# Kernel optimization log

Measured on AMD Instinct MI355X. Metric: run time of the kernel, lower is better.

The kernel has to match this reference:

```python
import jax, jax.numpy as jnp
import numpy as np

B, H, W, C = 32, 64, 64, 256
NH, WS, SHIFT = 8, 8, 4
HD = C // NH
N = WS * WS           # tokens per window
NW = (H // WS) * (W // WS)
HID = 4 * C
EPS_LN = 1e-5
LOGIT_MAX = float(np.log(1.0 / 0.01))


def _rel_coords_table():
    ch = np.arange(-(WS - 1), WS, dtype=np.float32)
    t = np.stack(np.meshgrid(ch, ch, indexing='ij'), axis=-1)  # (2WS-1, 2WS-1, 2)
    t = t / (WS - 1) * 8.0
    t = np.sign(t) * np.log2(np.abs(t) + 1.0) / np.log2(8.0)
    return t.reshape(-1, 2)  # ((2WS-1)^2, 2)


def _rel_pos_index():
    coords = np.stack(np.meshgrid(np.arange(WS), np.arange(WS), indexing='ij'))
    cf = coords.reshape(2, -1)
    rel = (cf[:, :, None] - cf[:, None, :]).transpose(1, 2, 0).copy()
    rel[:, :, 0] += WS - 1
    rel[:, :, 1] += WS - 1
    rel[:, :, 0] *= 2 * WS - 1
    return rel.sum(-1)  # (N, N) int


def _attn_mask():
    img = np.zeros((H, W), np.float32)
    cnt = 0
    for hs in (slice(0, -WS), slice(-WS, -SHIFT), slice(-SHIFT, None)):
        for ws in (slice(0, -WS), slice(-WS, -SHIFT), slice(-SHIFT, None)):
            img[hs, ws] = cnt
            cnt += 1
    mw = img.reshape(H // WS, WS, W // WS, WS).transpose(0, 2, 1, 3).reshape(-1, N)
    diff = mw[:, None, :] - mw[:, :, None]
    return np.where(diff != 0, -100.0, 0.0).astype(np.float32)  # (NW, N, N)


_RCT = jnp.asarray(_rel_coords_table())
_RPI = jnp.asarray(_rel_pos_index())
_MASK = jnp.asarray(_attn_mask())


def _ln(x, g, b):
    mu = jnp.mean(x, axis=-1, keepdims=True)
    var = jnp.mean(jnp.square(x - mu), axis=-1, keepdims=True)
    return (x - mu) * jax.lax.rsqrt(var + EPS_LN) * g + b


def _l2n(x):
    return x / jnp.sqrt(jnp.maximum(jnp.sum(x * x, axis=-1, keepdims=True), 1e-12))


def setup_inputs() -> dict:
    key = jax.random.key(0)
    ks = jax.random.split(key, 16)
    s = 0.02
    return {
        'x': jax.random.normal(ks[0], (B, H * W, C), jnp.float32),
        'qkv_w': jax.random.normal(ks[1], (C, 3 * C), jnp.float32) * s,
        'q_bias': jnp.zeros((C,), jnp.float32),
        'v_bias': jnp.zeros((C,), jnp.float32),
        'logit_scale': jnp.full((NH, 1, 1), np.log(10.0), jnp.float32),
        'cpb_w1': jax.random.normal(ks[2], (2, 512), jnp.float32) * s,
        'cpb_b1': jnp.zeros((512,), jnp.float32),
        'cpb_w2': jax.random.normal(ks[3], (512, NH), jnp.float32) * s,
        'proj_w': jax.random.normal(ks[4], (C, C), jnp.float32) * s,
        'proj_b': jnp.zeros((C,), jnp.float32),
        'norm1_g': jnp.ones((C,), jnp.float32),
        'norm1_b': jnp.zeros((C,), jnp.float32),
        'fc1_w': jax.random.normal(ks[5], (C, HID), jnp.float32) * s,
        'fc1_b': jnp.zeros((HID,), jnp.float32),
        'fc2_w': jax.random.normal(ks[6], (HID, C), jnp.float32) * s,
        'fc2_b': jnp.zeros((C,), jnp.float32),
        'norm2_g': jnp.ones((C,), jnp.float32),
        'norm2_b': jnp.zeros((C,), jnp.float32),
    }


def reference(x, qkv_w, q_bias, v_bias, logit_scale, cpb_w1, cpb_b1, cpb_w2,
              proj_w, proj_b, norm1_g, norm1_b, fc1_w, fc1_b, fc2_w, fc2_b,
              norm2_g, norm2_b):
    shortcut = x
    xs = x.reshape(B, H, W, C)
    # cyclic shift
    xs = jnp.roll(xs, shift=(-SHIFT, -SHIFT), axis=(1, 2))
    # window partition -> (B*NW, N, C)
    xw = xs.reshape(B, H // WS, WS, W // WS, WS, C).transpose(0, 1, 3, 2, 4, 5)
    xw = xw.reshape(B * NW, N, C)

    # qkv projection (kernel without bias, then split q/v biases, k bias zero)
    qkv_bias = jnp.concatenate([q_bias, jnp.zeros_like(q_bias), v_bias], axis=0)
    qkv = xw @ qkv_w + qkv_bias
    qkv = qkv.reshape(B * NW, N, 3, NH, HD).transpose(2, 0, 3, 1, 4)
    q, k, v = qkv[0], qkv[1], qkv[2]  # (B*NW, NH, N, HD)

    # cosine attention
    attn = jnp.einsum('bhnd,bhmd->bhnm', _l2n(q), _l2n(k))
    scale = jnp.exp(jnp.minimum(logit_scale, LOGIT_MAX))  # (NH,1,1)
    attn = attn * scale

    # CPB-MLP relative position bias
    table = jax.nn.relu(_RCT @ cpb_w1 + cpb_b1) @ cpb_w2          # ((2WS-1)^2, NH)
    bias = table[_RPI]                                            # (N, N, NH)
    bias = 16.0 * jax.nn.sigmoid(bias.transpose(2, 0, 1))         # (NH, N, N)
    attn = attn + bias[None]

    # shifted-window mask
    attn = attn.reshape(B, NW, NH, N, N) + _MASK[None, :, None]
    attn = jax.nn.softmax(attn.reshape(B * NW, NH, N, N), axis=-1)

    out = jnp.einsum('bhnm,bhmd->bhnd', attn, v)
    out = out.transpose(0, 2, 1, 3).reshape(B * NW, N, C)
    out = out @ proj_w + proj_b

    # window reverse + reverse shift
    out = out.reshape(B, H // WS, W // WS, WS, WS, C).transpose(0, 1, 3, 2, 4, 5)
    out = out.reshape(B, H, W, C)
    out = jnp.roll(out, shift=(SHIFT, SHIFT), axis=(1, 2)).reshape(B, H * W, C)

    # SwinV2 post-norm residuals
    x = shortcut + _ln(out, norm1_g, norm1_b)
    h = jax.nn.gelu(x @ fc1_w + fc1_b, approximate=False) @ fc2_w + fc2_b
    x = x + _ln(h, norm2_g, norm2_b)
    return x
```

## Files before the change

### kernel.cpp

```cpp
#include <hip/hip_runtime.h>


#define TOKS 131072
#define LOGIT_MAX 4.60517018598809136804f

typedef __attribute__((ext_vector_type(8))) short short8;
typedef __attribute__((ext_vector_type(4))) float f32x4;

__device__ __forceinline__ float b2f(unsigned short s) {
    union { unsigned int u; float f; } x; x.u = ((unsigned int)s) << 16; return x.f;
}
__device__ __forceinline__ unsigned short f2b(float f) {
    union { float f; unsigned int u; } x; x.f = f;
    unsigned int r = x.u + 0x7fffu + ((x.u >> 16) & 1u);
    return (unsigned short)(r >> 16);
}

#define MFMA16(a, b, c) __builtin_amdgcn_mfma_f32_16x16x32_bf16((a), (b), (c), 0, 0, 0)

#define GLOAD_LDS16(g, l)                                                      \
    __builtin_amdgcn_global_load_lds(                                          \
        (const __attribute__((address_space(1))) void*)(g),                    \
        (__attribute__((address_space(3))) void*)(l), 16, 0, 0)


__global__ __launch_bounds__(256) void cvt_kernel(const float* __restrict__ in,
                                                  unsigned short* __restrict__ out, int n) {
    int i = (blockIdx.x * 256 + threadIdx.x) * 4;
    if (i >= n) return;
    float4 v = *(const float4*)(in + i);
    ushort4 o;
    o.x = f2b(v.x); o.y = f2b(v.y); o.z = f2b(v.z); o.w = f2b(v.w);
    *(ushort4*)(out + i) = o;
}

__global__ __launch_bounds__(256) void wt_kernel(const float* __restrict__ src,
                                                 unsigned short* __restrict__ dst,
                                                 int K, int N) {
    int idx = blockIdx.x * 256 + threadIdx.x;
    if (idx >= K * N) return;
    int n = idx / K, k = idx - n * K;
    dst[idx] = f2b(src[(size_t)k * N + n]);
}

__device__ __forceinline__ float cpb_coord(int d) {
    float t = (float)d * (8.0f / 7.0f);
    float a = log2f(fabsf(t) + 1.0f) * (1.0f / 3.0f);
    return t < 0.0f ? -a : a;
}

__global__ __launch_bounds__(256) void cpb_kernel(
    const float* __restrict__ w1, const float* __restrict__ b1, const float* __restrict__ w2,
    const float* __restrict__ qb, const float* __restrict__ vb,
    float* __restrict__ biasT, float* __restrict__ qkv_bias)
{
    __shared__ float tbl[225];
    int h = blockIdx.x, t = threadIdx.x;
    if (t < 225) {
        float r0 = cpb_coord(t / 15 - 7), r1 = cpb_coord(t % 15 - 7);
        float acc = 0.f;
        for (int j = 0; j < 512; ++j) {
            float hid = fmaxf(r0 * w1[j] + r1 * w1[512 + j] + b1[j], 0.f);
            acc += hid * w2[j * 8 + h];
        }
        tbl[t] = acc;
    }
    __syncthreads();
    for (int o = t; o < 4096; o += 256) {
        int i = o >> 6, j = o & 63;
        int idx = ((i >> 3) - (j >> 3) + 7) * 15 + ((i & 7) - (j & 7) + 7);
        biasT[h * 4096 + o] = 16.0f / (1.0f + __expf(-tbl[idx]));
    }
    if (h == 0)
        for (int n = t; n < 768; n += 256)
            qkv_bias[n] = n < 256 ? qb[n] : (n < 512 ? 0.f : vb[n - 512]);
}

template<int EPI>
__global__ __launch_bounds__(256) void gemm_bt(
    const unsigned short* __restrict__ A, const unsigned short* __restrict__ Bt,
    const float* __restrict__ bias, unsigned short* __restrict__ out,
    int M, int N, int K)
{
    __shared__ __align__(16) unsigned short sA[128 * 32];
    __shared__ __align__(16) unsigned short sB[128 * 32];
    const int tid = threadIdx.x;
    const int lane = tid & 63;
    const int wave = tid >> 6;
    const int wm = (wave >> 1) * 64, wn = (wave & 1) * 64;
    const int nwg = (int)(gridDim.x * gridDim.y);
    int flat = (int)(blockIdx.y * gridDim.x + blockIdx.x);
    flat = (flat & 7) * (nwg >> 3) + (flat >> 3);
    const int bx = flat % (int)gridDim.x;
    const int by = flat / (int)gridDim.x;
    const int m0 = by * 128, n0 = bx * 128;
    const int l15 = lane & 15, lq = lane >> 4;
    const int r0 = tid >> 2, c0 = (tid & 3) << 3;

    f32x4 acc[4][4] = {};
    const size_t arow0 = (size_t)(m0 + r0) * K + c0;
    const size_t arow1 = (size_t)(m0 + r0 + 64) * K + c0;
    const size_t brow0 = (size_t)(n0 + r0) * K + c0;
    const size_t brow1 = (size_t)(n0 + r0 + 64) * K + c0;
    unsigned short* dA0 = sA + wave * 512;
    unsigned short* dA1 = sA + 2048 + wave * 512;
    unsigned short* dB0 = sB + wave * 512;
    unsigned short* dB1 = sB + 2048 + wave * 512;

    for (int k0 = 0; k0 < K; k0 += 32) {
        GLOAD_LDS16(A + arow0 + k0, dA0);
        GLOAD_LDS16(A + arow1 + k0, dA1);
        GLOAD_LDS16(Bt + brow0 + k0, dB0);
        GLOAD_LDS16(Bt + brow1 + k0, dB1);
        __syncthreads();
        short8 af[4], bw[4];
        #pragma unroll
        for (int t = 0; t < 4; ++t) {
            af[t] = *(const short8*)&sA[(wm + t * 16 + l15) * 32 + lq * 8];
            bw[t] = *(const short8*)&sB[(wn + t * 16 + l15) * 32 + lq * 8];
        }
        #pragma unroll
        for (int tm = 0; tm < 4; ++tm)
            #pragma unroll
            for (int tn = 0; tn < 4; ++tn)
                acc[tm][tn] = MFMA16(af[tm], bw[tn], acc[tm][tn]);
        __syncthreads();
    }

    float bv[4];
    #pragma unroll
    for (int tn = 0; tn < 4; ++tn) bv[tn] = bias[n0 + wn + tn * 16 + l15];

    #pragma unroll
    for (int tm = 0; tm < 4; ++tm)
        #pragma unroll
        for (int tn = 0; tn < 4; ++tn)
            #pragma unroll
            for (int r = 0; r < 4; ++r) {
                int gm = m0 + wm + tm * 16 + lq * 4 + r;
                int gn = n0 + wn + tn * 16 + l15;
                float v = acc[tm][tn][r] + bv[tn];
                if constexpr (EPI == 2) {
                    float u = v * (1.5957691216057308f + 0.0713548162972754f * v * v);
                    v = v / (1.0f + __expf(-u));
                }
                if constexpr (EPI == 1) {
                    int s = gn >> 8, hd = gn & 255;
                    out[((size_t)(s * 8 + (hd >> 5)) * TOKS + gm) * 32 + (hd & 31)] = f2b(v);
                } else {
                    out[(size_t)gm * N + gn] = f2b(v);
                }
            }
}

template<int MODE>
__global__ __launch_bounds__(256) void gemm_ln(
    const unsigned short* __restrict__ A, const unsigned short* __restrict__ Bt,
    const float* __restrict__ bias,
    const float* __restrict__ residf, const unsigned short* __restrict__ residb,
    const float* __restrict__ lng, const float* __restrict__ lnb,
    unsigned short* __restrict__ outb, float* __restrict__ outf, int K)
{
    __shared__ __align__(16) unsigned short sA[64 * 32];
    __shared__ __align__(16) unsigned short sB[256 * 32];
    const int tid = threadIdx.x;
    const int lane = tid & 63;
    const int wave = tid >> 6;
    const int wn = wave * 64;
    const int m0 = blockIdx.x * 64;
    const int l15 = lane & 15, lq = lane >> 4;
    const int r0 = tid >> 2, c0 = (tid & 3) << 3;

    f32x4 acc[4][4] = {};
    const size_t arow = (size_t)(m0 + r0) * K + c0;
    const size_t brow = (size_t)r0 * K + c0;
    unsigned short* dA  = sA + wave * 512;
    unsigned short* dB0 = sB + wave * 512;
    unsigned short* dB1 = sB + 2048 + wave * 512;
    unsigned short* dB2 = sB + 4096 + wave * 512;
    unsigned short* dB3 = sB + 6144 + wave * 512;

    for (int k0 = 0; k0 < K; k0 += 32) {
        GLOAD_LDS16(A + arow + k0, dA);
        GLOAD_LDS16(Bt + brow + k0, dB0);
        GLOAD_LDS16(Bt + brow + (size_t)64 * K + k0, dB1);
        GLOAD_LDS16(Bt + brow + (size_t)128 * K + k0, dB2);
        GLOAD_LDS16(Bt + brow + (size_t)192 * K + k0, dB3);
        __syncthreads();
        short8 af[4], bw[4];
        #pragma unroll
        for (int t = 0; t < 4; ++t) {
            af[t] = *(const short8*)&sA[(t * 16 + l15) * 32 + lq * 8];
            bw[t] = *(const short8*)&sB[(wn + t * 16 + l15) * 32 + lq * 8];
        }
        #pragma unroll
        for (int tm = 0; tm < 4; ++tm)
            #pragma unroll
            for (int tn = 0; tn < 4; ++tn)
                acc[tm][tn] = MFMA16(af[tm], bw[tn], acc[tm][tn]);
        __syncthreads();
    }

    float bv[4], gv[4], ev[4];
    #pragma unroll
    for (int tn = 0; tn < 4; ++tn) {
        int gn = wn + tn * 16 + l15;
        bv[tn] = bias[gn]; gv[tn] = lng[gn]; ev[tn] = lnb[gn];
    }

    float* sums = (float*)sA;
    float* sqs  = (float*)sA + 256;
    #pragma unroll
    for (int tm = 0; tm < 4; ++tm)
        #pragma unroll
        for (int r = 0; r < 4; ++r) {
            int rl = tm * 16 + lq * 4 + r;
            float s = 0.f, q = 0.f;
            #pragma unroll
            for (int tn = 0; tn < 4; ++tn) {
                float v = acc[tm][tn][r] + bv[tn];
                s += v; q += v * v;
            }
            #pragma unroll
            for (int o = 1; o < 16; o <<= 1) { s += __shfl_xor(s, o); q += __shfl_xor(q, o); }
            if (l15 == 0) { sums[rl * 4 + wave] = s; sqs[rl * 4 + wave] = q; }
        }
    __syncthreads();

    #pragma unroll
    for (int tm = 0; tm < 4; ++tm)
        #pragma unroll
        for (int r = 0; r < 4; ++r) {
            int rl = tm * 16 + lq * 4 + r;
            float s = sums[rl * 4] + sums[rl * 4 + 1] + sums[rl * 4 + 2] + sums[rl * 4 + 3];
            float q = sqs[rl * 4] + sqs[rl * 4 + 1] + sqs[rl * 4 + 2] + sqs[rl * 4 + 3];
            float mu = s * (1.0f / 256.0f);
            float rs = rsqrtf(q * (1.0f / 256.0f) - mu * mu + 1e-5f);
            size_t rowo = (size_t)(m0 + rl) * 256;
            #pragma unroll
            for (int tn = 0; tn < 4; ++tn) {
                int gn = wn + tn * 16 + l15;
                float v = acc[tm][tn][r] + bv[tn];
                float nv = (v - mu) * rs * gv[tn] + ev[tn];
                if constexpr (MODE == 1)
                    outb[rowo + gn] = f2b(residf[rowo + gn] + nv);
                else
                    outf[rowo + gn] = b2f(residb[rowo + gn]) + nv;
            }
        }
}


__device__ __forceinline__ int regid(int wy, int wx, int t) {
    int y = wy * 8 + (t >> 3), x = wx * 8 + (t & 7);
    int ry = (y < 56) ? 0 : (y < 60 ? 1 : 2);
    int rx = (x < 56) ? 0 : (x < 60 ? 1 : 2);
    return ry * 3 + rx;
}

__device__ __forceinline__ void load_norm(const unsigned short* __restrict__ p,
                                          unsigned short* __restrict__ dst, int lane) {
    union U { uint4 u; unsigned short s[8]; };
    U ld[4];
    #pragma unroll
    for (int c = 0; c < 4; ++c) ld[c].u = *(const uint4*)(p + c * 8);
    float f[32]; float ss = 0.f;
    #pragma unroll
    for (int c = 0; c < 4; ++c)
        #pragma unroll
        for (int j = 0; j < 8; ++j) { float v = b2f(ld[c].s[j]); f[c * 8 + j] = v; ss += v * v; }
    float nrm = rsqrtf(fmaxf(ss, 1e-12f));
    #pragma unroll
    for (int c = 0; c < 4; ++c) {
        U st;
        #pragma unroll
        for (int j = 0; j < 8; ++j) st.s[j] = f2b(f[c * 8 + j] * nrm);
        *(uint4*)(dst + lane * 32 + c * 8) = st.u;
    }
}

__global__ __launch_bounds__(64) void attn_kernel(
    const unsigned short* __restrict__ qkv, const float* __restrict__ biasT,
    const float* __restrict__ ls, unsigned short* __restrict__ outb)
{
    __shared__ __align__(16) unsigned short sQ[64 * 32];
    __shared__ __align__(16) unsigned short sK[64 * 32];
    __shared__ __align__(16) unsigned short sV[64 * 32];
    __shared__ __align__(16) unsigned short sP[64 * 64];

    const int lane = threadIdx.x;
    const int h = blockIdx.x & 7;
    const int win = blockIdx.x >> 3;
    const int b = win >> 6;
    const int wy = (win >> 3) & 7, wx = win & 7;
    const int l15 = lane & 15, lq = lane >> 4;

    {
        int ty = lane >> 3, tx = lane & 7;
        int hh = (wy * 8 + ty + 4) & 63, ww = (wx * 8 + tx + 4) & 63;
        size_t tok = (size_t)b * 4096 + hh * 64 + ww;
        const size_t plane = (size_t)TOKS * 32;
        const unsigned short* qp = qkv + (size_t)h * plane + tok * 32;
        const unsigned short* kp = qkv + (size_t)(8 + h) * plane + tok * 32;
        const unsigned short* vp = qkv + (size_t)(16 + h) * plane + tok * 32;
        load_norm(qp, sQ, lane);
        load_norm(kp, sK, lane);
        #pragma unroll
        for (int c = 0; c < 4; ++c)
            *(uint4*)&sV[lane * 32 + c * 8] = *(const uint4*)(vp + c * 8);
    }
    __syncthreads();

    short8 aQ[4], bK[4];
    #pragma unroll
    for (int t = 0; t < 4; ++t) {
        aQ[t] = *(const short8*)&sQ[(t * 16 + l15) * 32 + lq * 8];
        bK[t] = *(const short8*)&sK[(t * 16 + l15) * 32 + lq * 8];
    }
    f32x4 acc[4][4] = {};
    #pragma unroll
    for (int tm = 0; tm < 4; ++tm)
        #pragma unroll
        for (int tn = 0; tn < 4; ++tn)
            acc[tm][tn] = MFMA16(aQ[tm], bK[tn], acc[tm][tn]);

    float scale = __expf(fminf(ls[h], LOGIT_MAX));

    #pragma unroll
    for (int tm = 0; tm < 4; ++tm)
        #pragma unroll
        for (int r = 0; r < 4; ++r) {
            int i = tm * 16 + lq * 4 + r;
            int ri = regid(wy, wx, i);
            float v[4];
            #pragma unroll
            for (int tn = 0; tn < 4; ++tn) {
                int j = tn * 16 + l15;
                float sc = acc[tm][tn][r] * scale + biasT[h * 4096 + i * 64 + j];
                if (ri != regid(wy, wx, j)) sc -= 100.f;
                v[tn] = sc;
            }
            float m = fmaxf(fmaxf(v[0], v[1]), fmaxf(v[2], v[3]));
            #pragma unroll
            for (int o = 1; o < 16; o <<= 1) m = fmaxf(m, __shfl_xor(m, o));
            float sum = 0.f;
            #pragma unroll
            for (int tn = 0; tn < 4; ++tn) { v[tn] = __expf(v[tn] - m); sum += v[tn]; }
            #pragma unroll
            for (int o = 1; o < 16; o <<= 1) sum += __shfl_xor(sum, o);
            float inv = 1.0f / sum;
            #pragma unroll
            for (int tn = 0; tn < 4; ++tn)
                sP[i * 64 + tn * 16 + l15] = f2b(v[tn] * inv);
        }
    __syncthreads();

    f32x4 accO[4][2] = {};
    #pragma unroll
    for (int ks = 0; ks < 2; ++ks) {
        short8 bV[2];
        #pragma unroll
        for (int tn = 0; tn < 2; ++tn)
            #pragma unroll
            for (int jj = 0; jj < 8; ++jj)
                bV[tn][jj] = (short)sV[(ks * 32 + lq * 8 + jj) * 32 + tn * 16 + l15];
        #pragma unroll
        for (int tm = 0; tm < 4; ++tm) {
            short8 aP = *(const short8*)&sP[(tm * 16 + l15) * 64 + ks * 32 + lq * 8];
            accO[tm][0] = MFMA16(aP, bV[0], accO[tm][0]);
            accO[tm][1] = MFMA16(aP, bV[1], accO[tm][1]);
        }
    }

    #pragma unroll
    for (int tm = 0; tm < 4; ++tm)
        #pragma unroll
        for (int r = 0; r < 4; ++r) {
            int i = tm * 16 + lq * 4 + r;
            int hh = (wy * 8 + (i >> 3) + 4) & 63, ww = (wx * 8 + (i & 7) + 4) & 63;
            size_t rowo = ((size_t)b * 4096 + hh * 64 + ww) * 256 + h * 32;
            outb[rowo + l15] = f2b(accO[tm][0][r]);
            outb[rowo + 16 + l15] = f2b(accO[tm][1][r]);
        }
}


extern "C" void kernel_launch(void* const* d_in, const int* in_sizes, int n_in,
                              void* d_out, int out_size, void* d_ws, size_t ws_size,
                              hipStream_t stream) {
    (void)in_sizes; (void)n_in; (void)out_size; (void)ws_size;
    const float* x      = (const float*)d_in[0];
    const float* qkv_w  = (const float*)d_in[1];
    const float* q_bias = (const float*)d_in[2];
    const float* v_bias = (const float*)d_in[3];
    const float* lscale = (const float*)d_in[4];
    const float* cpb_w1 = (const float*)d_in[5];
    const float* cpb_b1 = (const float*)d_in[6];
    const float* cpb_w2 = (const float*)d_in[7];
    const float* proj_w = (const float*)d_in[8];
    const float* proj_b = (const float*)d_in[9];
    const float* n1g    = (const float*)d_in[10];
    const float* n1b    = (const float*)d_in[11];
    const float* fc1_w  = (const float*)d_in[12];
    const float* fc1_b  = (const float*)d_in[13];
    const float* fc2_w  = (const float*)d_in[14];
    const float* fc2_b  = (const float*)d_in[15];
    const float* n2g    = (const float*)d_in[16];
    const float* n2b    = (const float*)d_in[17];

    char* ws = (char*)d_ws;
    unsigned short* R1 = (unsigned short*)(ws);
    unsigned short* R2 = (unsigned short*)(ws + 268435456);
    unsigned short* R3 = (unsigned short*)(ws + 335544320);
    unsigned short* qkv_wT = (unsigned short*)(ws + 402653184);
    unsigned short* proj_wT = (unsigned short*)(ws + 403046400);
    unsigned short* fc1_wT  = (unsigned short*)(ws + 403177472);
    unsigned short* fc2_wT  = (unsigned short*)(ws + 403701760);
    float* qkv_bias = (float*)(ws + 404226048);
    float* biasT    = (float*)(ws + 404229120);

    cvt_kernel<<<TOKS * 256 / 1024, 256, 0, stream>>>(x, R2, TOKS * 256);
    wt_kernel<<<(256 * 768 + 255) / 256, 256, 0, stream>>>(qkv_w, qkv_wT, 256, 768);
    wt_kernel<<<(256 * 256 + 255) / 256, 256, 0, stream>>>(proj_w, proj_wT, 256, 256);
    wt_kernel<<<(256 * 1024 + 255) / 256, 256, 0, stream>>>(fc1_w, fc1_wT, 256, 1024);
    wt_kernel<<<(1024 * 256 + 255) / 256, 256, 0, stream>>>(fc2_w, fc2_wT, 1024, 256);
    cpb_kernel<<<8, 256, 0, stream>>>(cpb_w1, cpb_b1, cpb_w2, q_bias, v_bias, biasT, qkv_bias);

    gemm_bt<1><<<dim3(6, TOKS / 128), 256, 0, stream>>>(R2, qkv_wT, qkv_bias, R1, TOKS, 768, 256);
    attn_kernel<<<16384, 64, 0, stream>>>(R1, biasT, lscale, R2);
    gemm_ln<1><<<TOKS / 64, 256, 0, stream>>>(R2, proj_wT, proj_b, x, nullptr,
                                              n1g, n1b, R3, nullptr, 256);
    gemm_bt<2><<<dim3(8, TOKS / 128), 256, 0, stream>>>(R3, fc1_wT, fc1_b, R1, TOKS, 1024, 256);
    gemm_ln<2><<<TOKS / 64, 256, 0, stream>>>(R1, fc2_wT, fc2_b, nullptr, R3,
                                              n2g, n2b, nullptr, (float*)d_out, 1024);
}
```

Before: 985.4 us.

## Double-buffer LDS in GEMM kernels to overlap global loads with MFMA

Both GEMM kernels now use two LDS buffers. The next K-tile is prefetched with global_load_lds while the current tile is computed, and explicit vmcnt/lgkmcnt waits plus barriers replace the two __syncthreads per iteration. The grid-x dimension becomes a template constant so the tile-swizzle division is done at compile time, and the GELU epilogue uses a fused negative exponent with a hardware reciprocal. LDS use doubles, which may reduce occupancy, and the hand-written waitcnt counts must match the number of loads issued per stage.

Result: faster. 927.1 us (-5.9%).

```diff
diff --git a/kernel.cpp b/kernel.cpp
--- a/kernel.cpp
+++ b/kernel.cpp
@@ -76,56 +76,71 @@
             qkv_bias[n] = n < 256 ? qb[n] : (n < 512 ? 0.f : vb[n - 512]);
 }
 
-template<int EPI>
+template<int EPI, int GX>
 __global__ __launch_bounds__(256) void gemm_bt(
     const unsigned short* __restrict__ A, const unsigned short* __restrict__ Bt,
     const float* __restrict__ bias, unsigned short* __restrict__ out,
     int M, int N, int K)
 {
-    __shared__ __align__(16) unsigned short sA[128 * 32];
-    __shared__ __align__(16) unsigned short sB[128 * 32];
+    __shared__ __align__(16) unsigned short sA[2][128 * 32];
+    __shared__ __align__(16) unsigned short sB[2][128 * 32];
     const int tid = threadIdx.x;
     const int lane = tid & 63;
     const int wave = tid >> 6;
     const int wm = (wave >> 1) * 64, wn = (wave & 1) * 64;
-    const int nwg = (int)(gridDim.x * gridDim.y);
-    int flat = (int)(blockIdx.y * gridDim.x + blockIdx.x);
+    const int nwg = GX * (int)gridDim.y;
+    int flat = (int)(blockIdx.y * GX + blockIdx.x);
     flat = (flat & 7) * (nwg >> 3) + (flat >> 3);
-    const int bx = flat % (int)gridDim.x;
-    const int by = flat / (int)gridDim.x;
+    const int bx = flat % GX;
+    const int by = flat / GX;
     const int m0 = by * 128, n0 = bx * 128;
     const int l15 = lane & 15, lq = lane >> 4;
     const int r0 = tid >> 2, c0 = (tid & 3) << 3;
 
+    const unsigned short* pA0 = A + (size_t)(m0 + r0) * K + c0;
+    const unsigned short* pA1 = A + (size_t)(m0 + r0 + 64) * K + c0;
+    const unsigned short* pB0 = Bt + (size_t)(n0 + r0) * K + c0;
+    const unsigned short* pB1 = Bt + (size_t)(n0 + r0 + 64) * K + c0;
+
+    auto stage = [&](int buf, int k0) {
+        unsigned short* a = &sA[buf][wave * 512];
+        unsigned short* b = &sB[buf][wave * 512];
+        GLOAD_LDS16(pA0 + k0, a);
+        GLOAD_LDS16(pA1 + k0, a + 2048);
+        GLOAD_LDS16(pB0 + k0, b);
+        GLOAD_LDS16(pB1 + k0, b + 2048);
+    };
+
     f32x4 acc[4][4] = {};
-    const size_t arow0 = (size_t)(m0 + r0) * K + c0;
-    const size_t arow1 = (size_t)(m0 + r0 + 64) * K + c0;
-    const size_t brow0 = (size_t)(n0 + r0) * K + c0;
-    const size_t brow1 = (size_t)(n0 + r0 + 64) * K + c0;
-    unsigned short* dA0 = sA + wave * 512;
-    unsigned short* dA1 = sA + 2048 + wave * 512;
-    unsigned short* dB0 = sB + wave * 512;
-    unsigned short* dB1 = sB + 2048 + wave * 512;
-
-    for (int k0 = 0; k0 < K; k0 += 32) {
-        GLOAD_LDS16(A + arow0 + k0, dA0);
-        GLOAD_LDS16(A + arow1 + k0, dA1);
-        GLOAD_LDS16(Bt + brow0 + k0, dB0);
-        GLOAD_LDS16(Bt + brow1 + k0, dB1);
-        __syncthreads();
+    auto compute = [&](int buf) {
         short8 af[4], bw[4];
         #pragma unroll
         for (int t = 0; t < 4; ++t) {
-            af[t] = *(const short8*)&sA[(wm + t * 16 + l15) * 32 + lq * 8];
-            bw[t] = *(const short8*)&sB[(wn + t * 16 + l15) * 32 + lq * 8];
+            af[t] = *(const short8*)&sA[buf][(wm + t * 16 + l15) * 32 + lq * 8];
+            bw[t] = *(const short8*)&sB[buf][(wn + t * 16 + l15) * 32 + lq * 8];
         }
         #pragma unroll
         for (int tm = 0; tm < 4; ++tm)
             #pragma unroll
             for (int tn = 0; tn < 4; ++tn)
                 acc[tm][tn] = MFMA16(af[tm], bw[tn], acc[tm][tn]);
-        __syncthreads();
-    }
+    };
+
+    const int nt = K >> 5;
+    stage(0, 0);
+    for (int t = 0; t < nt - 1; ++t) {
+        stage((t & 1) ^ 1, (t + 1) << 5);
+        asm volatile("s_waitcnt vmcnt(4)" ::: "memory");
+        __builtin_amdgcn_s_barrier();
+        asm volatile("" ::: "memory");
+        compute(t & 1);
+        asm volatile("s_waitcnt lgkmcnt(0)" ::: "memory");
+        __builtin_amdgcn_s_barrier();
+    }
+    asm volatile("s_waitcnt vmcnt(0)" ::: "memory");
+    __builtin_amdgcn_s_barrier();
+    asm volatile("" ::: "memory");
+    compute((nt - 1) & 1);
 
     float bv[4];
     #pragma unroll
@@ -141,8 +156,9 @@
                 int gn = n0 + wn + tn * 16 + l15;
                 float v = acc[tm][tn][r] + bv[tn];
                 if constexpr (EPI == 2) {
-                    float u = v * (1.5957691216057308f + 0.0713548162972754f * v * v);
-                    v = v / (1.0f + __expf(-u));
+                    float e = __expf(v * fmaf(-0.0713548162972754f, v * v,
+                                              -1.5957691216057308f));
+                    v = v * __builtin_amdgcn_rcpf(1.0f + e);
                 }
                 if constexpr (EPI == 1) {
                     int s = gn >> 8, hd = gn & 255;
@@ -161,8 +177,8 @@
     const float* __restrict__ lng, const float* __restrict__ lnb,
     unsigned short* __restrict__ outb, float* __restrict__ outf, int K)
 {
-    __shared__ __align__(16) unsigned short sA[64 * 32];
-    __shared__ __align__(16) unsigned short sB[256 * 32];
+    __shared__ __align__(16) unsigned short sA[2][64 * 32];
+    __shared__ __align__(16) unsigned short sB[2][256 * 32];
     const int tid = threadIdx.x;
     const int lane = tid & 63;
     const int wave = tid >> 6;
@@ -171,35 +187,54 @@
     const int l15 = lane & 15, lq = lane >> 4;
     const int r0 = tid >> 2, c0 = (tid & 3) << 3;
 
+    const unsigned short* pA  = A + (size_t)(m0 + r0) * K + c0;
+    const unsigned short* pB0 = Bt + (size_t)r0 * K + c0;
+    const unsigned short* pB1 = pB0 + (size_t)64 * K;
+    const unsigned short* pB2 = pB0 + (size_t)128 * K;
+    const unsigned short* pB3 = pB0 + (size_t)192 * K;
+
+    auto stage = [&](int buf, int k0) {
+        unsigned short* a = &sA[buf][wave * 512];
+        unsigned short* b = &sB[buf][wave * 512];
+        GLOAD_LDS16(pA + k0, a);
+        GLOAD_LDS16(pB0 + k0, b);
+        GLOAD_LDS16(pB1 + k0, b + 2048);
+        GLOAD_LDS16(pB2 + k0, b + 4096);
+        GLOAD_LDS16(pB3 + k0, b + 6144);
+    };
+
     f32x4 acc[4][4] = {};
-    const size_t arow = (size_t)(m0 + r0) * K + c0;
-    const size_t brow = (size_t)r0 * K + c0;
-    unsigned short* dA  = sA + wave * 512;
-    unsigned short* dB0 = sB + wave * 512;
-    unsigned short* dB1 = sB + 2048 + wave * 512;
-    unsigned short* dB2 = sB + 4096 + wave * 512;
-    unsigned short* dB3 = sB + 6144 + wave * 512;
-
-    for (int k0 = 0; k0 < K; k0 += 32) {
-        GLOAD_LDS16(A + arow + k0, dA);
-        GLOAD_LDS16(Bt + brow + k0, dB0);
-        GLOAD_LDS16(Bt + brow + (size_t)64 * K + k0, dB1);
-        GLOAD_LDS16(Bt + brow + (size_t)128 * K + k0, dB2);
-        GLOAD_LDS16(Bt + brow + (size_t)192 * K + k0, dB3);
-        __syncthreads();
+    auto compute = [&](int buf) {
         short8 af[4], bw[4];
         #pragma unroll
         for (int t = 0; t < 4; ++t) {
-            af[t] = *(const short8*)&sA[(t * 16 + l15) * 32 + lq * 8];
-            bw[t] = *(const short8*)&sB[(wn + t * 16 + l15) * 32 + lq * 8];
+            af[t] = *(const short8*)&sA[buf][(t * 16 + l15) * 32 + lq * 8];
+            bw[t] = *(const short8*)&sB[buf][(wn + t * 16 + l15) * 32 + lq * 8];
         }
         #pragma unroll
         for (int tm = 0; tm < 4; ++tm)
             #pragma unroll
             for (int tn = 0; tn < 4; ++tn)
                 acc[tm][tn] = MFMA16(af[tm], bw[tn], acc[tm][tn]);
-        __syncthreads();
-    }
+    };
+
+    const int nt = K >> 5;
+    stage(0, 0);
+    for (int t = 0; t < nt - 1; ++t) {
+        stage((t & 1) ^ 1, (t + 1) << 5);
+        asm volatile("s_waitcnt vmcnt(5)" ::: "memory");
+        __builtin_amdgcn_s_barrier();
+        asm volatile("" ::: "memory");
+        compute(t & 1);
+        asm volatile("s_waitcnt lgkmcnt(0)" ::: "memory");
+        __builtin_amdgcn_s_barrier();
+    }
+    asm volatile("s_waitcnt vmcnt(0)" ::: "memory");
+    __builtin_amdgcn_s_barrier();
+    asm volatile("" ::: "memory");
+    compute((nt - 1) & 1);
+    asm volatile("s_waitcnt lgkmcnt(0)" ::: "memory");
+    __builtin_amdgcn_s_barrier();
 
     float bv[4], gv[4], ev[4];
     #pragma unroll
@@ -208,8 +243,8 @@
         bv[tn] = bias[gn]; gv[tn] = lng[gn]; ev[tn] = lnb[gn];
     }
 
-    float* sums = (float*)sA;
-    float* sqs  = (float*)sA + 256;
+    float* sums = (float*)&sA[0][0];
+    float* sqs  = (float*)&sA[0][0] + 256;
     #pragma unroll
     for (int tm = 0; tm < 4; ++tm)
         #pragma unroll
@@ -426,11 +461,11 @@
     wt_kernel<<<(1024 * 256 + 255) / 256, 256, 0, stream>>>(fc2_w, fc2_wT, 1024, 256);
     cpb_kernel<<<8, 256, 0, stream>>>(cpb_w1, cpb_b1, cpb_w2, q_bias, v_bias, biasT, qkv_bias);
 
-    gemm_bt<1><<<dim3(6, TOKS / 128), 256, 0, stream>>>(R2, qkv_wT, qkv_bias, R1, TOKS, 768, 256);
+    gemm_bt<1, 6><<<dim3(6, TOKS / 128), 256, 0, stream>>>(R2, qkv_wT, qkv_bias, R1, TOKS, 768, 256);
     attn_kernel<<<16384, 64, 0, stream>>>(R1, biasT, lscale, R2);
     gemm_ln<1><<<TOKS / 64, 256, 0, stream>>>(R2, proj_wT, proj_b, x, nullptr,
                                               n1g, n1b, R3, nullptr, 256);
-    gemm_bt<2><<<dim3(8, TOKS / 128), 256, 0, stream>>>(R3, fc1_wT, fc1_b, R1, TOKS, 1024, 256);
+    gemm_bt<2, 8><<<dim3(8, TOKS / 128), 256, 0, stream>>>(R3, fc1_wT, fc1_b, R1, TOKS, 1024, 256);
     gemm_ln<2><<<TOKS / 64, 256, 0, stream>>>(R1, fc2_wT, fc2_b, nullptr, R3,
                                               n2g, n2b, nullptr, (float*)d_out, 1024);
 }
```

## Load GEMM fragments directly from global into registers with double buffering

Applied to the files above, without the earlier changes.

Both GEMM kernels stop staging A and B tiles through LDS with global_load_lds and barriers. Each lane now loads its MFMA fragments straight from global memory into registers, double-buffered across two k-steps so the next loads overlap the current MFMAs. K and grid width become template constants, and the GELU epilogue uses a fused exp plus a fast reciprocal. The risk is redundant global and L2 traffic, since waves sharing rows or columns each fetch them separately, plus higher register pressure.

Result: slower. 1.263 ms (+28.1%).

```diff
diff --git a/kernel.cpp b/kernel.cpp
--- a/kernel.cpp
+++ b/kernel.cpp
@@ -17,11 +17,6 @@
 }
 
 #define MFMA16(a, b, c) __builtin_amdgcn_mfma_f32_16x16x32_bf16((a), (b), (c), 0, 0, 0)
-
-#define GLOAD_LDS16(g, l)                                                      \
-    __builtin_amdgcn_global_load_lds(                                          \
-        (const __attribute__((address_space(1))) void*)(g),                    \
-        (__attribute__((address_space(3))) void*)(l), 16, 0, 0)
 
 
 __global__ __launch_bounds__(256) void cvt_kernel(const float* __restrict__ in,
@@ -76,55 +71,68 @@
             qkv_bias[n] = n < 256 ? qb[n] : (n < 512 ? 0.f : vb[n - 512]);
 }
 
-template<int EPI>
+template<int EPI, int GX, int KT>
 __global__ __launch_bounds__(256) void gemm_bt(
     const unsigned short* __restrict__ A, const unsigned short* __restrict__ Bt,
-    const float* __restrict__ bias, unsigned short* __restrict__ out,
-    int M, int N, int K)
+    const float* __restrict__ bias, unsigned short* __restrict__ out, int N)
 {
-    __shared__ __align__(16) unsigned short sA[128 * 32];
-    __shared__ __align__(16) unsigned short sB[128 * 32];
+    constexpr int NT = KT >> 5;
     const int tid = threadIdx.x;
     const int lane = tid & 63;
     const int wave = tid >> 6;
     const int wm = (wave >> 1) * 64, wn = (wave & 1) * 64;
-    const int nwg = (int)(gridDim.x * gridDim.y);
-    int flat = (int)(blockIdx.y * gridDim.x + blockIdx.x);
+    const int nwg = GX * (int)gridDim.y;
+    int flat = (int)(blockIdx.y * GX + blockIdx.x);
     flat = (flat & 7) * (nwg >> 3) + (flat >> 3);
-    const int bx = flat % (int)gridDim.x;
-    const int by = flat / (int)gridDim.x;
+    const int bx = flat % GX;
+    const int by = flat / GX;
     const int m0 = by * 128, n0 = bx * 128;
     const int l15 = lane & 15, lq = lane >> 4;
-    const int r0 = tid >> 2, c0 = (tid & 3) << 3;
+
+    const unsigned short* pA[4];
+    const unsigned short* pB[4];
+    #pragma unroll
+    for (int f = 0; f < 4; ++f) {
+        pA[f] = A + (size_t)(m0 + wm + f * 16 + l15) * KT + lq * 8;
+        pB[f] = Bt + (size_t)(n0 + wn + f * 16 + l15) * KT + lq * 8;
+    }
+
+    short8 a0[4], b0[4], a1[4], b1[4];
+    #pragma unroll
+    for (int f = 0; f < 4; ++f) {
+        a0[f] = *(const short8*)(pA[f]);      b0[f] = *(const short8*)(pB[f]);
+        a1[f] = *(const short8*)(pA[f] + 32); b1[f] = *(const short8*)(pB[f] + 32);
+    }
 
     f32x4 acc[4][4] = {};
-    const size_t arow0 = (size_t)(m0 + r0) * K + c0;
-    const size_t arow1 = (size_t)(m0 + r0 + 64) * K + c0;
-    const size_t brow0 = (size_t)(n0 + r0) * K + c0;
-    const size_t brow1 = (size_t)(n0 + r0 + 64) * K + c0;
-    unsigned short* dA0 = sA + wave * 512;
-    unsigned short* dA1 = sA + 2048 + wave * 512;
-    unsigned short* dB0 = sB + wave * 512;
-    unsigned short* dB1 = sB + 2048 + wave * 512;
-
-    for (int k0 = 0; k0 < K; k0 += 32) {
-        GLOAD_LDS16(A + arow0 + k0, dA0);
-        GLOAD_LDS16(A + arow1 + k0, dA1);
-        GLOAD_LDS16(Bt + brow0 + k0, dB0);
-        GLOAD_LDS16(Bt + brow1 + k0, dB1);
-        __syncthreads();
-        short8 af[4], bw[4];
-        #pragma unroll
-        for (int t = 0; t < 4; ++t) {
-            af[t] = *(const short8*)&sA[(wm + t * 16 + l15) * 32 + lq * 8];
-            bw[t] = *(const short8*)&sB[(wn + t * 16 + l15) * 32 + lq * 8];
-        }
+    auto mfmas = [&](short8 (&a)[4], short8 (&b)[4]) {
         #pragma unroll
         for (int tm = 0; tm < 4; ++tm)
             #pragma unroll
             for (int tn = 0; tn < 4; ++tn)
-                acc[tm][tn] = MFMA16(af[tm], bw[tn], acc[tm][tn]);
-        __syncthreads();
+                acc[tm][tn] = MFMA16(a[tm], b[tn], acc[tm][tn]);
+    };
+
+    #pragma unroll 1
+    for (int t = 0; t < NT; t += 2) {
+        mfmas(a0, b0);
+        if (t + 2 < NT) {
+            #pragma unroll
+            for (int f = 0; f < 4; ++f) {
+                a0[f] = *(const short8*)(pA[f] + 64);
+                b0[f] = *(const short8*)(pB[f] + 64);
+            }
+        }
+        mfmas(a1, b1);
+        if (t + 3 < NT) {
+            #pragma unroll
+            for (int f = 0; f < 4; ++f) {
+                a1[f] = *(const short8*)(pA[f] + 96);
+                b1[f] = *(const short8*)(pB[f] + 96);
+            }
+        }
+        #pragma unroll
+        for (int f = 0; f < 4; ++f) { pA[f] += 64; pB[f] += 64; }
     }
 
     float bv[4];
@@ -141,8 +149,9 @@
                 int gn = n0 + wn + tn * 16 + l15;
                 float v = acc[tm][tn][r] + bv[tn];
                 if constexpr (EPI == 2) {
-                    float u = v * (1.5957691216057308f + 0.0713548162972754f * v * v);
-                    v = v / (1.0f + __expf(-u));
+                    float e = __expf(v * fmaf(-0.0713548162972754f, v * v,
+                                              -1.5957691216057308f));
+                    v = v * __builtin_amdgcn_rcpf(1.0f + e);
                 }
                 if constexpr (EPI == 1) {
                     int s = gn >> 8, hd = gn & 255;
@@ -153,52 +162,68 @@
             }
 }
 
-template<int MODE>
+template<int MODE, int KT>
 __global__ __launch_bounds__(256) void gemm_ln(
     const unsigned short* __restrict__ A, const unsigned short* __restrict__ Bt,
     const float* __restrict__ bias,
     const float* __restrict__ residf, const unsigned short* __restrict__ residb,
     const float* __restrict__ lng, const float* __restrict__ lnb,
-    unsigned short* __restrict__ outb, float* __restrict__ outf, int K)
+    unsigned short* __restrict__ outb, float* __restrict__ outf)
 {
-    __shared__ __align__(16) unsigned short sA[64 * 32];
-    __shared__ __align__(16) unsigned short sB[256 * 32];
+    constexpr int NT = KT >> 5;
+    __shared__ float sums[256];
+    __shared__ float sqs[256];
     const int tid = threadIdx.x;
     const int lane = tid & 63;
     const int wave = tid >> 6;
     const int wn = wave * 64;
     const int m0 = blockIdx.x * 64;
     const int l15 = lane & 15, lq = lane >> 4;
-    const int r0 = tid >> 2, c0 = (tid & 3) << 3;
+
+    const unsigned short* pA[4];
+    const unsigned short* pB[4];
+    #pragma unroll
+    for (int f = 0; f < 4; ++f) {
+        pA[f] = A + (size_t)(m0 + f * 16 + l15) * KT + lq * 8;
+        pB[f] = Bt + (size_t)(wn + f * 16 + l15) * KT + lq * 8;
+    }
+
+    short8 a0[4], b0[4], a1[4], b1[4];
+    #pragma unroll
+    for (int f = 0; f < 4; ++f) {
+        a0[f] = *(const short8*)(pA[f]);      b0[f] = *(const short8*)(pB[f]);
+        a1[f] = *(const short8*)(pA[f] + 32); b1[f] = *(const short8*)(pB[f] + 32);
+    }
 
     f32x4 acc[4][4] = {};
-    const size_t arow = (size_t)(m0 + r0) * K + c0;
-    const size_t brow = (size_t)r0 * K + c0;
-    unsigned short* dA  = sA + wave * 512;
-    unsigned short* dB0 = sB + wave * 512;
-    unsigned short* dB1 = sB + 2048 + wave * 512;
-    unsigned short* dB2 = sB + 4096 + wave * 512;
-    unsigned short* dB3 = sB + 6144 + wave * 512;
-
-    for (int k0 = 0; k0 < K; k0 += 32) {
-        GLOAD_LDS16(A + arow + k0, dA);
-        GLOAD_LDS16(Bt + brow + k0, dB0);
-        GLOAD_LDS16(Bt + brow + (size_t)64 * K + k0, dB1);
-        GLOAD_LDS16(Bt + brow + (size_t)128 * K + k0, dB2);
-        GLOAD_LDS16(Bt + brow + (size_t)192 * K + k0, dB3);
-        __syncthreads();
-        short8 af[4], bw[4];
-        #pragma unroll
-        for (int t = 0; t < 4; ++t) {
-            af[t] = *(const short8*)&sA[(t * 16 + l15) * 32 + lq * 8];
-            bw[t] = *(const short8*)&sB[(wn + t * 16 + l15) * 32 + lq * 8];
-        }
+    auto mfmas = [&](short8 (&a)[4], short8 (&b)[4]) {
         #pragma unroll
         for (int tm = 0; tm < 4; ++tm)
             #pragma unroll
             for (int tn = 0; tn < 4; ++tn)
-                acc[tm][tn] = MFMA16(af[tm], bw[tn], acc[tm][tn]);
-        __syncthreads();
+                acc[tm][tn] = MFMA16(a[tm], b[tn], acc[tm][tn]);
+    };
+
+    #pragma unroll 1
+    for (int t = 0; t < NT; t += 2) {
+        mfmas(a0, b0);
+        if (t + 2 < NT) {
+            #pragma unroll
+            for (int f = 0; f < 4; ++f) {
+                a0[f] = *(const short8*)(pA[f] + 64);
+                b0[f] = *(const short8*)(pB[f] + 64);
+            }
+        }
+        mfmas(a1, b1);
+        if (t + 3 < NT) {
+            #pragma unroll
+            for (int f = 0; f < 4; ++f) {
+                a1[f] = *(const short8*)(pA[f] + 96);
+                b1[f] = *(const short8*)(pB[f] + 96);
+            }
+        }
+        #pragma unroll
+        for (int f = 0; f < 4; ++f) { pA[f] += 64; pB[f] += 64; }
     }
 
     float bv[4], gv[4], ev[4];
@@ -208,8 +233,6 @@
         bv[tn] = bias[gn]; gv[tn] = lng[gn]; ev[tn] = lnb[gn];
     }
 
-    float* sums = (float*)sA;
-    float* sqs  = (float*)sA + 256;
     #pragma unroll
     for (int tm = 0; tm < 4; ++tm)
         #pragma unroll
@@ -426,11 +449,11 @@
     wt_kernel<<<(1024 * 256 + 255) / 256, 256, 0, stream>>>(fc2_w, fc2_wT, 1024, 256);
     cpb_kernel<<<8, 256, 0, stream>>>(cpb_w1, cpb_b1, cpb_w2, q_bias, v_bias, biasT, qkv_bias);
 
-    gemm_bt<1><<<dim3(6, TOKS / 128), 256, 0, stream>>>(R2, qkv_wT, qkv_bias, R1, TOKS, 768, 256);
+    gemm_bt<1, 6, 256><<<dim3(6, TOKS / 128), 256, 0, stream>>>(R2, qkv_wT, qkv_bias, R1, 768);
     attn_kernel<<<16384, 64, 0, stream>>>(R1, biasT, lscale, R2);
-    gemm_ln<1><<<TOKS / 64, 256, 0, stream>>>(R2, proj_wT, proj_b, x, nullptr,
-                                              n1g, n1b, R3, nullptr, 256);
-    gemm_bt<2><<<dim3(8, TOKS / 128), 256, 0, stream>>>(R3, fc1_wT, fc1_b, R1, TOKS, 1024, 256);
-    gemm_ln<2><<<TOKS / 64, 256, 0, stream>>>(R1, fc2_wT, fc2_b, nullptr, R3,
-                                              n2g, n2b, nullptr, (float*)d_out, 1024);
-}
+    gemm_ln<1, 256><<<TOKS / 64, 256, 0, stream>>>(R2, proj_wT, proj_b, x, nullptr,
+                                                   n1g, n1b, R3, nullptr);
+    gemm_bt<2, 8, 256><<<dim3(8, TOKS / 128), 256, 0, stream>>>(R3, fc1_wT, fc1_b, R1, 1024);
+    gemm_ln<2, 1024><<<TOKS / 64, 256, 0, stream>>>(R1, fc2_wT, fc2_b, nullptr, R3,
+                                                    n2g, n2b, nullptr, (float*)d_out);
+}
```
